# Optimization experiments

Measured on AMD Instinct MI355X. Metric: run time of the kernel, lower is better.

Reference implementation:

```python
import jax, jax.numpy as jnp
import numpy as np

N = 50000
E = 625000
D = 128
L = 3
BN_EPS = 1e-5


def setup_inputs() -> dict:
    key = jax.random.key(0)
    ks = jax.random.split(key, 12)
    x = jax.random.normal(ks[0], (N, D), dtype=jnp.float32)
    edge_index = jax.random.randint(ks[1], (2, E), 0, N, dtype=jnp.int64)
    s = 1.0 / np.sqrt(D)
    W1 = jax.random.uniform(ks[2], (L, D, D), jnp.float32, -s, s)
    b1 = jax.random.uniform(ks[3], (L, D), jnp.float32, -s, s)
    W2 = jax.random.uniform(ks[4], (L, D, D), jnp.float32, -s, s)
    b2 = jax.random.uniform(ks[5], (L, D), jnp.float32, -s, s)
    eps = jnp.zeros((L,), jnp.float32)  # GINConv train_eps init 0
    gamma = jnp.ones((L, D), jnp.float32)
    beta = jnp.zeros((L, D), jnp.float32)
    Wl = jax.random.uniform(ks[6], (L, D, D), jnp.float32, -s, s)
    bl = jax.random.uniform(ks[7], (L, D), jnp.float32, -s, s)
    return {"x": x, "edge_index": edge_index, "W1": W1, "b1": b1, "W2": W2,
            "b2": b2, "eps": eps, "gamma": gamma, "beta": beta, "Wl": Wl, "bl": bl}


def reference(x, edge_index, W1, b1, W2, b2, eps, gamma, beta, Wl, bl):
    src, dst = edge_index[0], edge_index[1]
    xs = [x]
    h = x
    for i in range(L):
        # GIN aggregation: sum of neighbor (source) features at target nodes
        agg = jax.ops.segment_sum(h[src], dst, num_segments=N)  # [N, D]
        z = (1.0 + eps[i]) * h + agg
        # MLP: Linear -> ReLU -> Linear
        z = jax.nn.relu(z @ W1[i] + b1[i]) @ W2[i] + b2[i]
        # BatchNorm1d (training mode: batch stats, biased variance)
        mu = jnp.mean(z, axis=0)
        var = jnp.mean((z - mu) ** 2, axis=0)
        z = gamma[i] * (z - mu) * jax.lax.rsqrt(var + BN_EPS) + beta[i]
        if i != 0:
            z = z + xs[-1]
        h = jax.nn.relu(z)
        xs.append(h)
    outs = [xs[i + 1] @ Wl[i] + bl[i] for i in range(L)]
    return jnp.concatenate(outs, axis=-1)  # [N, L*D]
```

## Files before the change

### kernel.cpp

```cpp
#include <hip/hip_runtime.h>
#include <hip/hip_bf16.h>
#include <stdint.h>

#define NN 50000
#define NE 625000
#define DD 128
#define NL 3
#define GB 391

typedef __bf16 bf16x8 __attribute__((ext_vector_type(8)));
typedef float f32x4 __attribute__((ext_vector_type(4)));

__device__ __forceinline__ float bflo(uint32_t u) { return __uint_as_float(u << 16); }
__device__ __forceinline__ float bfhi(uint32_t u) { return __uint_as_float(u & 0xffff0000u); }
__device__ __forceinline__ uint16_t f2bf(float f) {
    __hip_bfloat16 h = __float2bfloat16(f);
    return __builtin_bit_cast(uint16_t, h);
}
__device__ __forceinline__ uint32_t pack2(float lo, float hi) {
    return (uint32_t)f2bf(lo) | ((uint32_t)f2bf(hi) << 16);
}

__global__ void k_hist(const int* __restrict__ dstv, int* __restrict__ deg) {
    int e = blockIdx.x * 256 + threadIdx.x;
    if (e < NE) atomicAdd(&deg[dstv[e]], 1);
}

__global__ __launch_bounds__(512) void k_scan1(int* __restrict__ cursor ,
                                               int* __restrict__ rowptr,
                                               int* __restrict__ rowend,
                                               int* __restrict__ gcount) {
    __shared__ int s[512];
    __shared__ int base;
    int t = threadIdx.x;
    int i = blockIdx.x * 512 + t;
    int v = (i < NN) ? cursor[i] : 0;
    s[t] = v;
    __syncthreads();
    for (int st = 1; st < 512; st <<= 1) {
        int a = (t >= st) ? s[t - st] : 0;
        __syncthreads();
        s[t] += a;
        __syncthreads();
    }
    if (t == 511) base = atomicAdd(gcount, s[511]);
    __syncthreads();
    if (i < NN) {
        int b = base + s[t] - v;
        rowptr[i] = b;
        rowend[i] = b + v;
        cursor[i] = b;
    }
}

__global__ void k_fill(const int* __restrict__ srcv, const int* __restrict__ dstv,
                       int* __restrict__ cursor, int* __restrict__ colv) {
    int e = blockIdx.x * 256 + threadIdx.x;
    if (e < NE) {
        int d = dstv[e];
        int p = atomicAdd(&cursor[d], 1);
        colv[p] = srcv[e];
    }
}

#define WCONV_BLOCKS 576
__global__ void k_prep(const float* __restrict__ x, uint16_t* __restrict__ hb,
                       int* __restrict__ cursor, int* __restrict__ gcount,
                       const float* __restrict__ W1, const float* __restrict__ W2,
                       const float* __restrict__ Wl, uint16_t* __restrict__ Wb) {
    int b = blockIdx.x;
    if (b < WCONV_BLOCKS) {
        int id = b * 256 + threadIdx.x;
        int m = id >> 14;
        int r = id & 16383;
        int k = r >> 7;
        int col = r & 127;
        const float* src;
        if (m < 3) src = W1 + m * 16384;
        else if (m < 6) src = W2 + (m - 3) * 16384;
        else src = Wl + (m - 6) * 16384;
        float v = src[k * 128 + col];
        Wb[m * 16384 + col * 128 + (k ^ ((col & 7) << 3))] = f2bf(v);
        return;
    }
    int id = (b - WCONV_BLOCKS) * 256 + threadIdx.x;
    if (id == 0) *gcount = 0;
    if (id < NN) cursor[id] = 0;
    int base = id * 4;
    if (base >= NN * DD) return;
    float4 v = *(const float4*)(x + base);
    uint2 st;
    st.x = pack2(v.x, v.y);
    st.y = pack2(v.z, v.w);
    *(uint2*)(hb + base) = st;
}

#define ACC8(u) \
    a0 += bflo(u.x); a1 += bfhi(u.x); a2 += bflo(u.y); a3 += bfhi(u.y); \
    a4 += bflo(u.z); a5 += bfhi(u.z); a6 += bflo(u.w); a7 += bfhi(u.w);

__global__ __launch_bounds__(256) void k_agg(const uint16_t* __restrict__ hb,
                                             const int* __restrict__ rowptr,
                                             const int* __restrict__ rowend,
                                             const int* __restrict__ colv,
                                             const float* __restrict__ epsp, int layer,
                                             uint16_t* __restrict__ zb,
                                             float* __restrict__ bnsum) {
    if (blockIdx.x == 0) bnsum[threadIdx.x] = 0.f;
    int g = (blockIdx.x * 256 + threadIdx.x) >> 4;
    int l16 = threadIdx.x & 15;
    if (g >= NN) return;
    float onepe = 1.0f + epsp[layer];
    int beg = rowptr[g], end = rowend[g];
    const uint4* hp = (const uint4*)hb;
    float a0 = 0.f, a1 = 0.f, a2 = 0.f, a3 = 0.f, a4 = 0.f, a5 = 0.f, a6 = 0.f, a7 = 0.f;
    int j = beg;
    for (; j + 7 < end; j += 8) {
        int s0 = colv[j];
        int s1 = colv[j + 1];
        int s2 = colv[j + 2];
        int s3 = colv[j + 3];
        int s4 = colv[j + 4];
        int s5 = colv[j + 5];
        int s6 = colv[j + 6];
        int s7 = colv[j + 7];
        uint4 u0 = hp[(size_t)s0 * 16 + l16];
        uint4 u1 = hp[(size_t)s1 * 16 + l16];
        uint4 u2 = hp[(size_t)s2 * 16 + l16];
        uint4 u3 = hp[(size_t)s3 * 16 + l16];
        uint4 u4 = hp[(size_t)s4 * 16 + l16];
        uint4 u5 = hp[(size_t)s5 * 16 + l16];
        uint4 u6 = hp[(size_t)s6 * 16 + l16];
        uint4 u7 = hp[(size_t)s7 * 16 + l16];
        ACC8(u0) ACC8(u1) ACC8(u2) ACC8(u3)
        ACC8(u4) ACC8(u5) ACC8(u6) ACC8(u7)
    }
    for (; j + 3 < end; j += 4) {
        int s0 = colv[j];
        int s1 = colv[j + 1];
        int s2 = colv[j + 2];
        int s3 = colv[j + 3];
        uint4 u0 = hp[(size_t)s0 * 16 + l16];
        uint4 u1 = hp[(size_t)s1 * 16 + l16];
        uint4 u2 = hp[(size_t)s2 * 16 + l16];
        uint4 u3 = hp[(size_t)s3 * 16 + l16];
        ACC8(u0) ACC8(u1) ACC8(u2) ACC8(u3)
    }
    for (; j < end; ++j) {
        int s0 = colv[j];
        uint4 u = hp[(size_t)s0 * 16 + l16];
        ACC8(u)
    }
    uint4 hu = hp[(size_t)g * 16 + l16];
    a0 = fmaf(onepe, bflo(hu.x), a0); a1 = fmaf(onepe, bfhi(hu.x), a1);
    a2 = fmaf(onepe, bflo(hu.y), a2); a3 = fmaf(onepe, bfhi(hu.y), a3);
    a4 = fmaf(onepe, bflo(hu.z), a4); a5 = fmaf(onepe, bfhi(hu.z), a5);
    a6 = fmaf(onepe, bflo(hu.w), a6); a7 = fmaf(onepe, bfhi(hu.w), a7);
    uint4 st;
    st.x = pack2(a0, a1); st.y = pack2(a2, a3);
    st.z = pack2(a4, a5); st.w = pack2(a6, a7);
    ((uint4*)zb)[(size_t)g * 16 + l16] = st;
}

__global__ __launch_bounds__(256) void k_mlp(const uint16_t* __restrict__ A,
                                             const uint16_t* __restrict__ W1img,
                                             const uint16_t* __restrict__ W2img,
                                             const float* __restrict__ b1,
                                             const float* __restrict__ b2,
                                             float* __restrict__ bnsum,
                                             uint16_t* __restrict__ z2b) {
    __shared__ uint16_t ldsW[16384];
    __shared__ uint16_t ldsT[16384];
    int tid = threadIdx.x;
    int wid = tid >> 6, lane = tid & 63;

    bf16x8 w2r[8];
#pragma unroll
    for (int it = 0; it < 8; ++it) w2r[it] = *(const bf16x8*)(W2img + (it * 256 + tid) * 8);

#pragma unroll
    for (int it = 0; it < 8; ++it) {
        int idx = (it * 256 + tid) * 8;
        *(bf16x8*)(&ldsW[idx]) = *(const bf16x8*)(W1img + idx);
    }
    __syncthreads();

    const int brow = blockIdx.x * 128;
    const int m0 = wid * 32;
    const int l15 = lane & 15;
    const int lhi = lane >> 4;

    f32x4 acc[2][8];
    f32x4 zero = {0.f, 0.f, 0.f, 0.f};
#pragma unroll
    for (int m = 0; m < 2; ++m)
#pragma unroll
        for (int n = 0; n < 8; ++n) acc[m][n] = zero;

    const char* Ab = (const char*)A;
#pragma unroll
    for (int kk = 0; kk < 4; ++kk) {
        int kbyte = kk * 64 + (lhi << 4);
        bf16x8 afrag[2];
#pragma unroll
        for (int m = 0; m < 2; ++m) {
            int row = brow + m0 + m * 16 + l15;
            if (row >= NN) row = NN - 1;
            afrag[m] = *(const bf16x8*)(Ab + (size_t)row * 256 + kbyte);
        }
#pragma unroll
        for (int n = 0; n < 8; ++n) {
            int col = n * 16 + l15;
            int addr = col * 256 + (kbyte ^ ((col & 7) << 4));
            bf16x8 bfrag = *(const bf16x8*)((const char*)ldsW + addr);
            acc[0][n] = __builtin_amdgcn_mfma_f32_16x16x32_bf16(afrag[0], bfrag, acc[0][n], 0, 0, 0);
            acc[1][n] = __builtin_amdgcn_mfma_f32_16x16x32_bf16(afrag[1], bfrag, acc[1][n], 0, 0, 0);
        }
    }

    {
        float bc[8];
#pragma unroll
        for (int n = 0; n < 8; ++n) bc[n] = b1[n * 16 + l15];
#pragma unroll
        for (int m = 0; m < 2; ++m) {
            int rbase = m0 + m * 16 + (lhi << 2);
#pragma unroll
            for (int r = 0; r < 4; ++r) {
                int row = rbase + r;
#pragma unroll
                for (int n = 0; n < 8; ++n) {
                    float v = fmaxf(acc[m][n][r] + bc[n], 0.f);
                    int col = n * 16 + l15;
                    int byteoff = row * 256 + ((col * 2) ^ ((row & 7) << 4));
                    *(uint16_t*)((char*)ldsT + byteoff) = f2bf(v);
                }
            }
        }
    }
    __syncthreads();

#pragma unroll
    for (int it = 0; it < 8; ++it) *(bf16x8*)(&ldsW[(it * 256 + tid) * 8]) = w2r[it];
    __syncthreads();

#pragma unroll
    for (int m = 0; m < 2; ++m)
#pragma unroll
        for (int n = 0; n < 8; ++n) acc[m][n] = zero;

#pragma unroll
    for (int kk = 0; kk < 4; ++kk) {
        int kbyte = kk * 64 + (lhi << 4);
        bf16x8 afrag[2];
#pragma unroll
        for (int m = 0; m < 2; ++m) {
            int rowl = m0 + m * 16 + l15;
            afrag[m] = *(const bf16x8*)((const char*)ldsT + rowl * 256 + (kbyte ^ ((rowl & 7) << 4)));
        }
#pragma unroll
        for (int n = 0; n < 8; ++n) {
            int col = n * 16 + l15;
            int addr = col * 256 + (kbyte ^ ((col & 7) << 4));
            bf16x8 bfrag = *(const bf16x8*)((const char*)ldsW + addr);
            acc[0][n] = __builtin_amdgcn_mfma_f32_16x16x32_bf16(afrag[0], bfrag, acc[0][n], 0, 0, 0);
            acc[1][n] = __builtin_amdgcn_mfma_f32_16x16x32_bf16(afrag[1], bfrag, acc[1][n], 0, 0, 0);
        }
    }

    float bc2[8];
#pragma unroll
    for (int n = 0; n < 8; ++n) bc2[n] = b2[n * 16 + l15];

    float s1[8], s2[8];
#pragma unroll
    for (int n = 0; n < 8; ++n) { s1[n] = 0.f; s2[n] = 0.f; }

#pragma unroll
    for (int m = 0; m < 2; ++m) {
        int rbase = brow + m0 + m * 16 + (lhi << 2);
#pragma unroll
        for (int r = 0; r < 4; ++r) {
            int row = rbase + r;
            bool ok = row < NN;
#pragma unroll
            for (int n = 0; n < 8; ++n) {
                float v = acc[m][n][r] + bc2[n];
                if (ok) {
                    z2b[(size_t)row * 128 + n * 16 + l15] = f2bf(v);
                    s1[n] += v;
                    s2[n] += v * v;
                }
            }
        }
    }

    __syncthreads();
    float* ls = (float*)ldsT;
    ls[tid] = 0.f;
    __syncthreads();
#pragma unroll
    for (int n = 0; n < 8; ++n) {
        float a1 = s1[n] + __shfl_xor(s1[n], 16);
        a1 += __shfl_xor(a1, 32);
        float a2 = s2[n] + __shfl_xor(s2[n], 16);
        a2 += __shfl_xor(a2, 32);
        if (lane < 16) {
            atomicAdd(&ls[n * 16 + lane], a1);
            atomicAdd(&ls[128 + n * 16 + lane], a2);
        }
    }
    __syncthreads();
    atomicAdd(&bnsum[tid], ls[tid]);
}

__global__ __launch_bounds__(256) void k_apply(const uint16_t* __restrict__ z2b,
                                               const uint16_t* __restrict__ hin,
                                               const float* __restrict__ bnsum,
                                               const float* __restrict__ gamma,
                                               const float* __restrict__ beta, int layer,
                                               uint16_t* __restrict__ hout) {
    __shared__ float sA[128], sB[128];
    int tid = threadIdx.x;
    if (tid < 128) {
        float mu = bnsum[tid] * (1.0f / NN);
        float var = bnsum[128 + tid] * (1.0f / NN) - mu * mu;
        float a = gamma[layer * 128 + tid] * rsqrtf(var + 1e-5f);
        sA[tid] = a;
        sB[tid] = beta[layer * 128 + tid] - mu * a;
    }
    __syncthreads();
    int id = blockIdx.x * 256 + tid;
    int base = id * 4;
    if (base >= NN * DD) return;
    int c = base & 127;
    uint2 zu = *(const uint2*)(z2b + base);
    float4 av = *(const float4*)(sA + c);
    float4 bv = *(const float4*)(sB + c);
    float v0 = fmaf(av.x, bflo(zu.x), bv.x);
    float v1 = fmaf(av.y, bfhi(zu.x), bv.y);
    float v2 = fmaf(av.z, bflo(zu.y), bv.z);
    float v3 = fmaf(av.w, bfhi(zu.y), bv.w);
    if (layer > 0) {
        uint2 h = *(const uint2*)(hin + base);
        v0 += bflo(h.x);
        v1 += bfhi(h.x);
        v2 += bflo(h.y);
        v3 += bfhi(h.y);
    }
    v0 = fmaxf(v0, 0.f);
    v1 = fmaxf(v1, 0.f);
    v2 = fmaxf(v2, 0.f);
    v3 = fmaxf(v3, 0.f);
    uint2 st;
    st.x = pack2(v0, v1);
    st.y = pack2(v2, v3);
    *(uint2*)(hout + base) = st;
}

__global__ __launch_bounds__(256) void k_outgemm(const uint16_t* __restrict__ h1,
                                                 const uint16_t* __restrict__ h2,
                                                 const uint16_t* __restrict__ h3,
                                                 const uint16_t* __restrict__ Wb6,
                                                 const float* __restrict__ bl,
                                                 float* __restrict__ out) {
    __shared__ uint16_t lds[16384];
    int layer = blockIdx.x / GB;
    int blk = blockIdx.x - layer * GB;
    const uint16_t* A = (layer == 0) ? h1 : ((layer == 1) ? h2 : h3);
    const uint16_t* Wimg = Wb6 + layer * 16384;
    const float* bias = bl + layer * 128;

    int tid = threadIdx.x;
    int wid = tid >> 6, lane = tid & 63;
#pragma unroll
    for (int it = 0; it < 8; ++it) {
        int idx = (it * 256 + tid) * 8;
        bf16x8 v = *(const bf16x8*)(Wimg + idx);
        *(bf16x8*)(&lds[idx]) = v;
    }
    __syncthreads();

    const int brow = blk * 128;
    const int m0 = wid * 32;
    const int l15 = lane & 15;
    const int lhi = lane >> 4;

    f32x4 acc[2][8];
    f32x4 zero = {0.f, 0.f, 0.f, 0.f};
#pragma unroll
    for (int m = 0; m < 2; ++m)
#pragma unroll
        for (int n = 0; n < 8; ++n) acc[m][n] = zero;

    const char* Ab = (const char*)A;
#pragma unroll
    for (int kk = 0; kk < 4; ++kk) {
        int kbyte = kk * 64 + (lhi << 4);
        bf16x8 afrag[2];
#pragma unroll
        for (int m = 0; m < 2; ++m) {
            int row = brow + m0 + m * 16 + l15;
            if (row >= NN) row = NN - 1;
            afrag[m] = *(const bf16x8*)(Ab + (size_t)row * 256 + kbyte);
        }
#pragma unroll
        for (int n = 0; n < 8; ++n) {
            int col = n * 16 + l15;
            int addr = col * 256 + (kbyte ^ ((col & 7) << 4));
            bf16x8 bfrag = *(const bf16x8*)((const char*)lds + addr);
            acc[0][n] = __builtin_amdgcn_mfma_f32_16x16x32_bf16(afrag[0], bfrag, acc[0][n], 0, 0, 0);
            acc[1][n] = __builtin_amdgcn_mfma_f32_16x16x32_bf16(afrag[1], bfrag, acc[1][n], 0, 0, 0);
        }
    }

    float bcol[8];
#pragma unroll
    for (int n = 0; n < 8; ++n) bcol[n] = bias[n * 16 + l15];

#pragma unroll
    for (int m = 0; m < 2; ++m) {
        int rbase = brow + m0 + m * 16 + (lhi << 2);
#pragma unroll
        for (int r = 0; r < 4; ++r) {
            int row = rbase + r;
            if (row < NN) {
#pragma unroll
                for (int n = 0; n < 8; ++n) {
                    float v = acc[m][n][r] + bcol[n];
                    out[(size_t)row * (NL * DD) + layer * 128 + n * 16 + l15] = v;
                }
            }
        }
    }
}

extern "C" void kernel_launch(void* const* d_in, const int* in_sizes, int n_in,
                              void* d_out, int out_size, void* d_ws, size_t ws_size,
                              hipStream_t stream) {
    const float* x = (const float*)d_in[0];
    const int* ei = (const int*)d_in[1];
    const float* W1 = (const float*)d_in[2];
    const float* b1 = (const float*)d_in[3];
    const float* W2 = (const float*)d_in[4];
    const float* b2 = (const float*)d_in[5];
    const float* epsp = (const float*)d_in[6];
    const float* gamma = (const float*)d_in[7];
    const float* beta = (const float*)d_in[8];
    const float* Wl = (const float*)d_in[9];
    const float* bl = (const float*)d_in[10];
    float* out = (float*)d_out;

    char* w = (char*)d_ws;
    size_t off = 0;
    auto take = [&](size_t b) -> char* {
        char* p = w + off;
        off += (b + 255) & ~(size_t)255;
        return p;
    };
    uint16_t* hb[4];
    for (int i = 0; i < 4; ++i) hb[i] = (uint16_t*)take((size_t)NN * DD * 2);
    uint16_t* zb = (uint16_t*)take((size_t)NN * DD * 2);
    uint16_t* z2b = (uint16_t*)take((size_t)NN * DD * 2);
    int* rowptr = (int*)take((size_t)NN * 4);
    int* rowend = (int*)take((size_t)NN * 4);
    int* cursor = (int*)take((size_t)NN * 4);
    int* colv = (int*)take((size_t)NE * 4);
    uint16_t* Wb = (uint16_t*)take(9 * 16384 * 2);
    float* bnsum = (float*)take(256 * 4);
    int* gcount = (int*)take(256);

    const int* srcv = ei;
    const int* dstv = ei + NE;

    const int x2bf_blocks = (NN * DD / 4 + 255) / 256;
    k_prep<<<WCONV_BLOCKS + x2bf_blocks, 256, 0, stream>>>(x, hb[0], cursor, gcount,
                                                           W1, W2, Wl, Wb);

    k_hist<<<(NE + 255) / 256, 256, 0, stream>>>(dstv, cursor);
    k_scan1<<<98, 512, 0, stream>>>(cursor, rowptr, rowend, gcount);
    k_fill<<<(NE + 255) / 256, 256, 0, stream>>>(srcv, dstv, cursor, colv);

    const int agg_blocks = (NN * 16 + 255) / 256;

    for (int l = 0; l < NL; ++l) {
        k_agg<<<agg_blocks, 256, 0, stream>>>(hb[l], rowptr, rowend, colv, epsp, l, zb, bnsum);
        k_mlp<<<GB, 256, 0, stream>>>(zb, Wb + l * 16384, Wb + (3 + l) * 16384,
                                      b1 + l * 128, b2 + l * 128, bnsum, z2b);
        k_apply<<<x2bf_blocks, 256, 0, stream>>>(z2b, hb[l], bnsum, gamma, beta,
                                                 l, hb[l + 1]);
    }
    k_outgemm<<<NL * GB, 256, 0, stream>>>(hb[1], hb[2], hb[3], Wb + 6 * 16384, bl, out);
}
```

Baseline: 266.2 us.

## Hoist A-fragment loads before weight staging, widen apply, drop 8-way gather unroll

```diff
diff --git a/kernel.cpp b/kernel.cpp
--- a/kernel.cpp
+++ b/kernel.cpp
@@ -66,6 +66,7 @@
 #define WCONV_BLOCKS 576
 __global__ void k_prep(const float* __restrict__ x, uint16_t* __restrict__ hb,
                        int* __restrict__ cursor, int* __restrict__ gcount,
+                       float* __restrict__ bnsum,
                        const float* __restrict__ W1, const float* __restrict__ W2,
                        const float* __restrict__ Wl, uint16_t* __restrict__ Wb) {
     int b = blockIdx.x;
@@ -85,6 +86,7 @@
     }
     int id = (b - WCONV_BLOCKS) * 256 + threadIdx.x;
     if (id == 0) *gcount = 0;
+    if (id < NL * 256) bnsum[id] = 0.f;
     if (id < NN) cursor[id] = 0;
     int base = id * 4;
     if (base >= NN * DD) return;
@@ -104,9 +106,7 @@
                                              const int* __restrict__ rowend,
                                              const int* __restrict__ colv,
                                              const float* __restrict__ epsp, int layer,
-                                             uint16_t* __restrict__ zb,
-                                             float* __restrict__ bnsum) {
-    if (blockIdx.x == 0) bnsum[threadIdx.x] = 0.f;
+                                             uint16_t* __restrict__ zb) {
     int g = (blockIdx.x * 256 + threadIdx.x) >> 4;
     int l16 = threadIdx.x & 15;
     if (g >= NN) return;
@@ -115,26 +115,6 @@
     const uint4* hp = (const uint4*)hb;
     float a0 = 0.f, a1 = 0.f, a2 = 0.f, a3 = 0.f, a4 = 0.f, a5 = 0.f, a6 = 0.f, a7 = 0.f;
     int j = beg;
-    for (; j + 7 < end; j += 8) {
-        int s0 = colv[j];
-        int s1 = colv[j + 1];
-        int s2 = colv[j + 2];
-        int s3 = colv[j + 3];
-        int s4 = colv[j + 4];
-        int s5 = colv[j + 5];
-        int s6 = colv[j + 6];
-        int s7 = colv[j + 7];
-        uint4 u0 = hp[(size_t)s0 * 16 + l16];
-        uint4 u1 = hp[(size_t)s1 * 16 + l16];
-        uint4 u2 = hp[(size_t)s2 * 16 + l16];
-        uint4 u3 = hp[(size_t)s3 * 16 + l16];
-        uint4 u4 = hp[(size_t)s4 * 16 + l16];
-        uint4 u5 = hp[(size_t)s5 * 16 + l16];
-        uint4 u6 = hp[(size_t)s6 * 16 + l16];
-        uint4 u7 = hp[(size_t)s7 * 16 + l16];
-        ACC8(u0) ACC8(u1) ACC8(u2) ACC8(u3)
-        ACC8(u4) ACC8(u5) ACC8(u6) ACC8(u7)
-    }
     for (; j + 3 < end; j += 4) {
         int s0 = colv[j];
         int s1 = colv[j + 1];
@@ -174,47 +154,52 @@
     int tid = threadIdx.x;
     int wid = tid >> 6, lane = tid & 63;
 
-    bf16x8 w2r[8];
-#pragma unroll
-    for (int it = 0; it < 8; ++it) w2r[it] = *(const bf16x8*)(W2img + (it * 256 + tid) * 8);
-
-#pragma unroll
-    for (int it = 0; it < 8; ++it) {
-        int idx = (it * 256 + tid) * 8;
-        *(bf16x8*)(&ldsW[idx]) = *(const bf16x8*)(W1img + idx);
-    }
-    __syncthreads();
-
     const int brow = blockIdx.x * 128;
     const int m0 = wid * 32;
     const int l15 = lane & 15;
     const int lhi = lane >> 4;
 
-    f32x4 acc[2][8];
-    f32x4 zero = {0.f, 0.f, 0.f, 0.f};
-#pragma unroll
-    for (int m = 0; m < 2; ++m)
-#pragma unroll
-        for (int n = 0; n < 8; ++n) acc[m][n] = zero;
-
+    bf16x8 afr[4][2];
     const char* Ab = (const char*)A;
 #pragma unroll
     for (int kk = 0; kk < 4; ++kk) {
         int kbyte = kk * 64 + (lhi << 4);
-        bf16x8 afrag[2];
 #pragma unroll
         for (int m = 0; m < 2; ++m) {
             int row = brow + m0 + m * 16 + l15;
             if (row >= NN) row = NN - 1;
-            afrag[m] = *(const bf16x8*)(Ab + (size_t)row * 256 + kbyte);
-        }
+            afr[kk][m] = *(const bf16x8*)(Ab + (size_t)row * 256 + kbyte);
+        }
+    }
+
+    bf16x8 w2r[8];
+#pragma unroll
+    for (int it = 0; it < 8; ++it) w2r[it] = *(const bf16x8*)(W2img + (it * 256 + tid) * 8);
+
+#pragma unroll
+    for (int it = 0; it < 8; ++it) {
+        int idx = (it * 256 + tid) * 8;
+        *(bf16x8*)(&ldsW[idx]) = *(const bf16x8*)(W1img + idx);
+    }
+    __syncthreads();
+
+    f32x4 acc[2][8];
+    f32x4 zero = {0.f, 0.f, 0.f, 0.f};
+#pragma unroll
+    for (int m = 0; m < 2; ++m)
+#pragma unroll
+        for (int n = 0; n < 8; ++n) acc[m][n] = zero;
+
+#pragma unroll
+    for (int kk = 0; kk < 4; ++kk) {
+        int kbyte = kk * 64 + (lhi << 4);
 #pragma unroll
         for (int n = 0; n < 8; ++n) {
             int col = n * 16 + l15;
             int addr = col * 256 + (kbyte ^ ((col & 7) << 4));
             bf16x8 bfrag = *(const bf16x8*)((const char*)ldsW + addr);
-            acc[0][n] = __builtin_amdgcn_mfma_f32_16x16x32_bf16(afrag[0], bfrag, acc[0][n], 0, 0, 0);
-            acc[1][n] = __builtin_amdgcn_mfma_f32_16x16x32_bf16(afrag[1], bfrag, acc[1][n], 0, 0, 0);
+            acc[0][n] = __builtin_amdgcn_mfma_f32_16x16x32_bf16(afr[kk][0], bfrag, acc[0][n], 0, 0, 0);
+            acc[1][n] = __builtin_amdgcn_mfma_f32_16x16x32_bf16(afr[kk][1], bfrag, acc[1][n], 0, 0, 0);
         }
     }
 
@@ -316,46 +301,46 @@
 
 __global__ __launch_bounds__(256) void k_apply(const uint16_t* __restrict__ z2b,
                                                const uint16_t* __restrict__ hin,
-                                               const float* __restrict__ bnsum,
-                                               const float* __restrict__ gamma,
-                                               const float* __restrict__ beta, int layer,
+                                               const float* __restrict__ bnsumL,
+                                               const float* __restrict__ gammal,
+                                               const float* __restrict__ betal, int has_skip,
                                                uint16_t* __restrict__ hout) {
     __shared__ float sA[128], sB[128];
     int tid = threadIdx.x;
     if (tid < 128) {
-        float mu = bnsum[tid] * (1.0f / NN);
-        float var = bnsum[128 + tid] * (1.0f / NN) - mu * mu;
-        float a = gamma[layer * 128 + tid] * rsqrtf(var + 1e-5f);
+        float mu = bnsumL[tid] * (1.0f / NN);
+        float var = bnsumL[128 + tid] * (1.0f / NN) - mu * mu;
+        float a = gammal[tid] * rsqrtf(var + 1e-5f);
         sA[tid] = a;
-        sB[tid] = beta[layer * 128 + tid] - mu * a;
-    }
-    __syncthreads();
-    int id = blockIdx.x * 256 + tid;
-    int base = id * 4;
-    if (base >= NN * DD) return;
-    int c = base & 127;
-    uint2 zu = *(const uint2*)(z2b + base);
-    float4 av = *(const float4*)(sA + c);
-    float4 bv = *(const float4*)(sB + c);
-    float v0 = fmaf(av.x, bflo(zu.x), bv.x);
-    float v1 = fmaf(av.y, bfhi(zu.x), bv.y);
-    float v2 = fmaf(av.z, bflo(zu.y), bv.z);
-    float v3 = fmaf(av.w, bfhi(zu.y), bv.w);
-    if (layer > 0) {
-        uint2 h = *(const uint2*)(hin + base);
-        v0 += bflo(h.x);
-        v1 += bfhi(h.x);
-        v2 += bflo(h.y);
-        v3 += bfhi(h.y);
-    }
-    v0 = fmaxf(v0, 0.f);
-    v1 = fmaxf(v1, 0.f);
-    v2 = fmaxf(v2, 0.f);
-    v3 = fmaxf(v3, 0.f);
-    uint2 st;
+        sB[tid] = betal[tid] - mu * a;
+    }
+    __syncthreads();
+    size_t base = ((size_t)blockIdx.x * 256 + tid) * 8;
+    int c = (int)(base & 127);
+    uint4 zu = *(const uint4*)(z2b + base);
+    float v0 = fmaf(sA[c + 0], bflo(zu.x), sB[c + 0]);
+    float v1 = fmaf(sA[c + 1], bfhi(zu.x), sB[c + 1]);
+    float v2 = fmaf(sA[c + 2], bflo(zu.y), sB[c + 2]);
+    float v3 = fmaf(sA[c + 3], bfhi(zu.y), sB[c + 3]);
+    float v4 = fmaf(sA[c + 4], bflo(zu.z), sB[c + 4]);
+    float v5 = fmaf(sA[c + 5], bfhi(zu.z), sB[c + 5]);
+    float v6 = fmaf(sA[c + 6], bflo(zu.w), sB[c + 6]);
+    float v7 = fmaf(sA[c + 7], bfhi(zu.w), sB[c + 7]);
+    if (has_skip) {
+        uint4 h = *(const uint4*)(hin + base);
+        v0 += bflo(h.x); v1 += bfhi(h.x);
+        v2 += bflo(h.y); v3 += bfhi(h.y);
+        v4 += bflo(h.z); v5 += bfhi(h.z);
+        v6 += bflo(h.w); v7 += bfhi(h.w);
+    }
+    v0 = fmaxf(v0, 0.f); v1 = fmaxf(v1, 0.f); v2 = fmaxf(v2, 0.f); v3 = fmaxf(v3, 0.f);
+    v4 = fmaxf(v4, 0.f); v5 = fmaxf(v5, 0.f); v6 = fmaxf(v6, 0.f); v7 = fmaxf(v7, 0.f);
+    uint4 st;
     st.x = pack2(v0, v1);
     st.y = pack2(v2, v3);
-    *(uint2*)(hout + base) = st;
+    st.z = pack2(v4, v5);
+    st.w = pack2(v6, v7);
+    *(uint4*)(hout + base) = st;
 }
 
 __global__ __launch_bounds__(256) void k_outgemm(const uint16_t* __restrict__ h1,
@@ -373,6 +358,24 @@
 
     int tid = threadIdx.x;
     int wid = tid >> 6, lane = tid & 63;
+    const int brow = blk * 128;
+    const int m0 = wid * 32;
+    const int l15 = lane & 15;
+    const int lhi = lane >> 4;
+
+    bf16x8 afr[4][2];
+    const char* Ab = (const char*)A;
+#pragma unroll
+    for (int kk = 0; kk < 4; ++kk) {
+        int kbyte = kk * 64 + (lhi << 4);
+#pragma unroll
+        for (int m = 0; m < 2; ++m) {
+            int row = brow + m0 + m * 16 + l15;
+            if (row >= NN) row = NN - 1;
+            afr[kk][m] = *(const bf16x8*)(Ab + (size_t)row * 256 + kbyte);
+        }
+    }
+
 #pragma unroll
     for (int it = 0; it < 8; ++it) {
         int idx = (it * 256 + tid) * 8;
@@ -381,11 +384,6 @@
     }
     __syncthreads();
 
-    const int brow = blk * 128;
-    const int m0 = wid * 32;
-    const int l15 = lane & 15;
-    const int lhi = lane >> 4;
-
     f32x4 acc[2][8];
     f32x4 zero = {0.f, 0.f, 0.f, 0.f};
 #pragma unroll
@@ -393,24 +391,16 @@
 #pragma unroll
         for (int n = 0; n < 8; ++n) acc[m][n] = zero;
 
-    const char* Ab = (const char*)A;
 #pragma unroll
     for (int kk = 0; kk < 4; ++kk) {
         int kbyte = kk * 64 + (lhi << 4);
-        bf16x8 afrag[2];
-#pragma unroll
-        for (int m = 0; m < 2; ++m) {
-            int row = brow + m0 + m * 16 + l15;
-            if (row >= NN) row = NN - 1;
-            afrag[m] = *(const bf16x8*)(Ab + (size_t)row * 256 + kbyte);
-        }
 #pragma unroll
         for (int n = 0; n < 8; ++n) {
             int col = n * 16 + l15;
             int addr = col * 256 + (kbyte ^ ((col & 7) << 4));
             bf16x8 bfrag = *(const bf16x8*)((const char*)lds + addr);
-            acc[0][n] = __builtin_amdgcn_mfma_f32_16x16x32_bf16(afrag[0], bfrag, acc[0][n], 0, 0, 0);
-            acc[1][n] = __builtin_amdgcn_mfma_f32_16x16x32_bf16(afrag[1], bfrag, acc[1][n], 0, 0, 0);
+            acc[0][n] = __builtin_amdgcn_mfma_f32_16x16x32_bf16(afr[kk][0], bfrag, acc[0][n], 0, 0, 0);
+            acc[1][n] = __builtin_amdgcn_mfma_f32_16x16x32_bf16(afr[kk][1], bfrag, acc[1][n], 0, 0, 0);
         }
     }
 
@@ -467,28 +457,30 @@
     int* cursor = (int*)take((size_t)NN * 4);
     int* colv = (int*)take((size_t)NE * 4);
     uint16_t* Wb = (uint16_t*)take(9 * 16384 * 2);
-    float* bnsum = (float*)take(256 * 4);
+    float* bnsum = (float*)take(NL * 256 * 4);
     int* gcount = (int*)take(256);
 
     const int* srcv = ei;
     const int* dstv = ei + NE;
 
-    const int x2bf_blocks = (NN * DD / 4 + 255) / 256;
-    k_prep<<<WCONV_BLOCKS + x2bf_blocks, 256, 0, stream>>>(x, hb[0], cursor, gcount,
-                                                           W1, W2, Wl, Wb);
+    const int prep_tail_blocks = (NN * DD / 4 + 255) / 256;
+    k_prep<<<WCONV_BLOCKS + prep_tail_blocks, 256, 0, stream>>>(x, hb[0], cursor, gcount, bnsum,
+                                                                W1, W2, Wl, Wb);
 
     k_hist<<<(NE + 255) / 256, 256, 0, stream>>>(dstv, cursor);
     k_scan1<<<98, 512, 0, stream>>>(cursor, rowptr, rowend, gcount);
     k_fill<<<(NE + 255) / 256, 256, 0, stream>>>(srcv, dstv, cursor, colv);
 
     const int agg_blocks = (NN * 16 + 255) / 256;
+    const int apply_blocks = NN * DD / 8 / 256;
 
     for (int l = 0; l < NL; ++l) {
-        k_agg<<<agg_blocks, 256, 0, stream>>>(hb[l], rowptr, rowend, colv, epsp, l, zb, bnsum);
+        k_agg<<<agg_blocks, 256, 0, stream>>>(hb[l], rowptr, rowend, colv, epsp, l, zb);
         k_mlp<<<GB, 256, 0, stream>>>(zb, Wb + l * 16384, Wb + (3 + l) * 16384,
-                                      b1 + l * 128, b2 + l * 128, bnsum, z2b);
-        k_apply<<<x2bf_blocks, 256, 0, stream>>>(z2b, hb[l], bnsum, gamma, beta,
-                                                 l, hb[l + 1]);
+                                      b1 + l * 128, b2 + l * 128, bnsum + l * 256, z2b);
+        k_apply<<<apply_blocks, 256, 0, stream>>>(z2b, hb[l], bnsum + l * 256,
+                                                  gamma + l * 128, beta + l * 128,
+                                                  l > 0 ? 1 : 0, hb[l + 1]);
     }
     k_outgemm<<<NL * GB, 256, 0, stream>>>(hb[1], hb[2], hb[3], Wb + 6 * 16384, bl, out);
 }
```

After: 260.2 us. -2.3%, faster.
